# Kernel optimization log

Hardware: AMD Instinct MI355X
Metric: run time of the kernel (lower is better)

Reference implementation:

```python
import jax, jax.numpy as jnp
import numpy as np

N_CHANNELS = 8
SECTION = 32768
F_IN = 64
F_OUT = 64
UNITS = 512


def setup_inputs() -> dict:
    key = jax.random.key(0)
    ks = jax.random.split(key, 10)
    scale = lambda fan_in: 1.0 / np.sqrt(fan_in)
    return {
        "x": jax.random.normal(ks[0], (N_CHANNELS * SECTION, F_IN), jnp.float32),
        "w0": jax.random.normal(ks[1], (N_CHANNELS, UNITS, F_IN), jnp.float32) * scale(F_IN),
        "w1": jax.random.normal(ks[2], (N_CHANNELS, UNITS, UNITS), jnp.float32) * scale(UNITS),
        "w2": jax.random.normal(ks[3], (N_CHANNELS, UNITS, UNITS), jnp.float32) * scale(UNITS),
        "w3": jax.random.normal(ks[4], (N_CHANNELS, F_OUT, UNITS), jnp.float32) * scale(UNITS),
        "b0": jax.random.normal(ks[5], (N_CHANNELS, UNITS), jnp.float32) * 0.01,
        "b1": jax.random.normal(ks[6], (N_CHANNELS, UNITS), jnp.float32) * 0.01,
        "b2": jax.random.normal(ks[7], (N_CHANNELS, UNITS), jnp.float32) * 0.01,
        "b3": jax.random.normal(ks[8], (N_CHANNELS, F_OUT), jnp.float32) * 0.01,
        "section_size": SECTION,
    }


def reference(x, w0, w1, w2, w3, b0, b1, b2, b3, section_size):
    # Equal sections of size `section_size` per channel: reshape to [C, S, F]
    # and run the per-channel MLP as batched (grouped) GEMMs.
    C = w0.shape[0]
    xs = x.reshape(C, section_size, -1)  # [C, S, F_in]
    for w, b in ((w0, b0), (w1, b1), (w2, b2)):
        xs = jax.nn.relu(jnp.einsum('csi,coi->cso', xs, w) + b[:, None, :])
    ys = jnp.einsum('csi,coi->cso', xs, w3) + b3[:, None, :]  # [C, S, F_out]
    return ys.reshape(C * section_size, -1)
```

## Files before the change

### kernel.cpp

```cpp
#include <hip/hip_runtime.h>
#include <hip/hip_bf16.h>

#define CH 8
#define SEC 32768
#define FIN 64
#define FOUT 64
#define UN 512
#define BM 64

typedef __bf16 bf16;
typedef bf16 bf16x8 __attribute__((ext_vector_type(8)));
typedef bf16 bf16x4 __attribute__((ext_vector_type(4)));
typedef float f32x4 __attribute__((ext_vector_type(4)));

__device__ __forceinline__ void gload_lds16(const void* g, void* l) {
  __builtin_amdgcn_global_load_lds(
      (const __attribute__((address_space(1))) void*)g,
      (__attribute__((address_space(3))) void*)l, 16, 0, 0);
}

template<int N>
__device__ __forceinline__ void wait_vmcnt() {
  asm volatile("s_waitcnt vmcnt(%0)" :: "i"(N) : "memory");
  __builtin_amdgcn_sched_barrier(0);
}

__device__ __forceinline__ bf16x8 cvt8(const float* __restrict__ src) {
  f32x4 u0 = *(const f32x4*)src;
  f32x4 u1 = *(const f32x4*)(src + 4);
  bf16x8 v;
  v[0] = (bf16)u0[0]; v[1] = (bf16)u0[1]; v[2] = (bf16)u0[2]; v[3] = (bf16)u0[3];
  v[4] = (bf16)u1[0]; v[5] = (bf16)u1[1]; v[6] = (bf16)u1[2]; v[7] = (bf16)u1[3];
  return v;
}

__device__ __forceinline__ void store_cvt8(void* dst, const float* __restrict__ src) {
  *(bf16x8*)dst = cvt8(src);
}

template<int K, bool WSPATH>
__device__ __forceinline__ void run_main_layer(
    const bf16* __restrict__ wb,
    const float* __restrict__ wf,
    const float* __restrict__ bias, char* __restrict__ act,
    char* __restrict__ wslot,
    int w, int l, int l15, int l4, int rot)
{
  constexpr int NKS = K / 32;
  constexpr int MASK = NKS - 1;
  const int col0 = w * 64;
  const char* abase = act + l * 16;

  f32x4 acc[4][4];
#pragma unroll
  for (int mt = 0; mt < 4; ++mt)
#pragma unroll
    for (int nt = 0; nt < 4; ++nt)
      acc[mt][nt] = f32x4{0.f, 0.f, 0.f, 0.f};

  if constexpr (WSPATH) {
    const bf16* gbase = wb + ((size_t)(w * 4) * NKS * 64 + l) * 8;

    auto stage = [&](int j, int soff) {
      const int ks = (j + rot) & MASK;
#pragma unroll
      for (int i = 0; i < 4; ++i)
        gload_lds16(gbase + (size_t)(i * NKS + ks) * 512, wslot + soff + i * 1024);
    };

    auto compute = [&](int j, int boff) {
      const int ks = (j + rot) & MASK;
      bf16x8 a[4], b[4];
#pragma unroll
      for (int nt = 0; nt < 4; ++nt)
        b[nt] = *(const bf16x8*)(wslot + boff + nt * 1024 + l * 16);
#pragma unroll
      for (int mt = 0; mt < 4; ++mt)
        a[mt] = *(const bf16x8*)(abase + (mt * NKS + ks) * 1024);
      __builtin_amdgcn_s_setprio(1);
#pragma unroll
      for (int mt = 0; mt < 4; ++mt)
#pragma unroll
        for (int nt = 0; nt < 4; ++nt)
          acc[mt][nt] = __builtin_amdgcn_mfma_f32_16x16x32_bf16(a[mt], b[nt], acc[mt][nt], 0, 0, 0);
      __builtin_amdgcn_s_setprio(0);
    };

    stage(0, 0);
    if constexpr (NKS > 1) stage(1, 4096);

    int soff = 8192, boff = 0;
    for (int j = 0; j + 2 < NKS; ++j) {
      stage(j + 2, soff);
      soff += 4096; if (soff == 12288) soff = 0;
      wait_vmcnt<8>();
      compute(j, boff);
      boff += 4096; if (boff == 12288) boff = 0;
    }
    if constexpr (NKS > 1) {
      wait_vmcnt<4>();
      compute(NKS - 2, ((NKS - 2) % 3) * 4096);
    }
    wait_vmcnt<0>();
    compute(NKS - 1, ((NKS - 1) % 3) * 4096);
  } else {
    const float* bpf[4];
#pragma unroll
    for (int nt = 0; nt < 4; ++nt)
      bpf[nt] = wf + (size_t)(col0 + nt * 16 + l15) * K + l4 * 8;
    for (int j = 0; j < NKS; ++j) {
      const int ks = (j + rot) & MASK;
      bf16x8 a[4], b[4];
#pragma unroll
      for (int nt = 0; nt < 4; ++nt) b[nt] = cvt8(bpf[nt] + ks * 32);
#pragma unroll
      for (int mt = 0; mt < 4; ++mt)
        a[mt] = *(const bf16x8*)(abase + (mt * NKS + ks) * 1024);
#pragma unroll
      for (int mt = 0; mt < 4; ++mt)
#pragma unroll
        for (int nt = 0; nt < 4; ++nt)
          acc[mt][nt] = __builtin_amdgcn_mfma_f32_16x16x32_bf16(a[mt], b[nt], acc[mt][nt], 0, 0, 0);
    }
  }

  __syncthreads();

#pragma unroll
  for (int nt = 0; nt < 4; ++nt) {
    const int col = col0 + nt * 16 + l15;
    const float bv = bias[col];
    const int base = (col >> 5) * 1024 + ((col >> 3) & 3) * 256 + (col & 7) * 2 + l4 * 64;
#pragma unroll
    for (int mt = 0; mt < 4; ++mt)
#pragma unroll
      for (int r = 0; r < 4; ++r) {
        float v = acc[mt][nt][r] + bv;
        v = v > 0.f ? v : 0.f;
        *(bf16*)(act + mt * 16384 + base + r * 16) = (bf16)v;
      }
  }
  __syncthreads();
}

template<bool WSPATH>
__device__ __forceinline__ void run_final_layer(
    const bf16* __restrict__ wb, const float* __restrict__ wf,
    const float* __restrict__ bias, const char* __restrict__ act,
    float* __restrict__ gout,
    int w, int l, int l15, int l4, int rot)
{
  constexpr int NKS = 16;
  const int mt = w >> 1;
  const int nb = (w & 1) * 2;
  const char* abase = act + mt * 16384 + l * 16;

  f32x4 acc[2];
  acc[0] = f32x4{0.f, 0.f, 0.f, 0.f};
  acc[1] = f32x4{0.f, 0.f, 0.f, 0.f};

  if constexpr (WSPATH) {
    const bf16* bp0 = wb + ((size_t)(nb + 0) * 16 * 64 + l) * 8;
    const bf16* bp1 = wb + ((size_t)(nb + 1) * 16 * 64 + l) * 8;
    bf16x8 B0[2], B1[2];
    B0[0] = *(const bf16x8*)(bp0 + (size_t)(rot & 15) * 512);
    B0[1] = *(const bf16x8*)(bp1 + (size_t)(rot & 15) * 512);
#pragma unroll
    for (int j = 0; j < NKS; j += 2) {
      {
        const int ksn = (j + 1 + rot) & 15;
        B1[0] = *(const bf16x8*)(bp0 + (size_t)ksn * 512);
        B1[1] = *(const bf16x8*)(bp1 + (size_t)ksn * 512);
        const int ks = (j + rot) & 15;
        const bf16x8 a = *(const bf16x8*)(abase + ks * 1024);
        acc[0] = __builtin_amdgcn_mfma_f32_16x16x32_bf16(a, B0[0], acc[0], 0, 0, 0);
        acc[1] = __builtin_amdgcn_mfma_f32_16x16x32_bf16(a, B0[1], acc[1], 0, 0, 0);
      }
      {
        if (j + 2 < NKS) {
          const int ksn = (j + 2 + rot) & 15;
          B0[0] = *(const bf16x8*)(bp0 + (size_t)ksn * 512);
          B0[1] = *(const bf16x8*)(bp1 + (size_t)ksn * 512);
        }
        const int ks = (j + 1 + rot) & 15;
        const bf16x8 a = *(const bf16x8*)(abase + ks * 1024);
        acc[0] = __builtin_amdgcn_mfma_f32_16x16x32_bf16(a, B1[0], acc[0], 0, 0, 0);
        acc[1] = __builtin_amdgcn_mfma_f32_16x16x32_bf16(a, B1[1], acc[1], 0, 0, 0);
      }
    }
  } else {
    const float* bpf0 = wf + (size_t)((nb + 0) * 16 + l15) * UN + l4 * 8;
    const float* bpf1 = wf + (size_t)((nb + 1) * 16 + l15) * UN + l4 * 8;
    for (int j = 0; j < NKS; ++j) {
      const int ks = (j + rot) & 15;
      const bf16x8 b0 = cvt8(bpf0 + ks * 32);
      const bf16x8 b1 = cvt8(bpf1 + ks * 32);
      const bf16x8 a = *(const bf16x8*)(abase + ks * 1024);
      acc[0] = __builtin_amdgcn_mfma_f32_16x16x32_bf16(a, b0, acc[0], 0, 0, 0);
      acc[1] = __builtin_amdgcn_mfma_f32_16x16x32_bf16(a, b1, acc[1], 0, 0, 0);
    }
  }

#pragma unroll
  for (int i = 0; i < 2; ++i) {
    const int col = (nb + i) * 16 + l15;
    const float bv = bias[col];
#pragma unroll
    for (int r = 0; r < 4; ++r)
      gout[(size_t)(mt * 16 + l4 * 4 + r) * FOUT + col] = acc[i][r] + bv;
  }
}

template<bool WSPATH>
__global__ __launch_bounds__(512, 2) void mlp_fused(
    const float* __restrict__ x,
    const float* __restrict__ w0f, const float* __restrict__ w1f,
    const float* __restrict__ w2f, const float* __restrict__ w3f,
    const float* __restrict__ b0, const float* __restrict__ b1,
    const float* __restrict__ b2, const float* __restrict__ b3,
    const bf16* __restrict__ wbase,
    float* __restrict__ out)
{
  extern __shared__ char smem[];
  char* act = smem;

  const int tid = threadIdx.x;
  const int w = tid >> 6, l = tid & 63;
  const int l15 = l & 15, l4 = l >> 4;
  char* wslot = smem + 65536 + w * 12288;

  const int wg = (blockIdx.x & 7) * 512 + (blockIdx.x >> 3);
  const int ch = wg >> 9;
  const int row0 = (wg & 511) * BM;
  const int rot = wg & 15;

  const bf16* w0b = wbase + (size_t)ch * UN * FIN;
  const bf16* w1b = wbase + CH * UN * FIN + (size_t)ch * UN * UN;
  const bf16* w2b = wbase + CH * UN * FIN + CH * UN * UN + (size_t)ch * UN * UN;
  const bf16* w3b = wbase + CH * UN * FIN + 2 * CH * UN * UN + (size_t)ch * FOUT * UN;
  const float* w0c = w0f + (size_t)ch * UN * FIN;
  const float* w1c = w1f + (size_t)ch * UN * UN;
  const float* w2c = w2f + (size_t)ch * UN * UN;
  const float* w3c = w3f + (size_t)ch * FOUT * UN;
  const float* b0c = b0 + ch * UN;
  const float* b1c = b1 + ch * UN;
  const float* b2c = b2 + ch * UN;
  const float* b3c = b3 + ch * FOUT;

  {
    const float* xs = x + (size_t)(ch * SEC + row0) * FIN;
    store_cvt8(act + w * 1024 + l * 16,
               xs + ((w >> 1) * 16 + l15) * FIN + (w & 1) * 32 + l4 * 8);
  }
  __syncthreads();

  run_main_layer<64,  WSPATH>(w0b, w0c, b0c, act, wslot, w, l, l15, l4, rot);
  run_main_layer<512, WSPATH>(w1b, w1c, b1c, act, wslot, w, l, l15, l4, rot);
  run_main_layer<512, WSPATH>(w2b, w2c, b2c, act, wslot, w, l, l15, l4, rot);
  run_final_layer<WSPATH>(w3b, w3c, b3c, act,
                          out + (size_t)(ch * SEC + row0) * FOUT,
                          w, l, l15, l4, rot);
}

template<int K, int N>
__device__ __forceinline__ void cvt_one(const float* __restrict__ src,
                                        bf16* __restrict__ dst, int t)
{
  constexpr int NKS = K / 32;
  constexpr int perCh = N * K / 8;
  const int ch = t / perCh;
  const int r = t - ch * perCh;
  const int l = r & 63;
  const int p = r >> 6;
  const int ks = p & (NKS - 1);
  const int f = p / NKS;
  const float* s = src + (size_t)ch * N * K + (size_t)(f * 16 + (l & 15)) * K
                 + ks * 32 + (l >> 4) * 8;
  store_cvt8(dst + (size_t)t * 8, s);
}

__global__ void cvt_weights(const float* __restrict__ w0, const float* __restrict__ w1,
                            const float* __restrict__ w2, const float* __restrict__ w3,
                            bf16* __restrict__ o)
{
  constexpr int T0 = CH * UN * FIN / 8;
  constexpr int T1 = CH * UN * UN / 8;
  constexpr int total = 2 * T0 + 2 * T1;
  for (int t = blockIdx.x * blockDim.x + threadIdx.x; t < total;
       t += gridDim.x * blockDim.x) {
    if (t < T0)                cvt_one<FIN, UN>(w0, o, t);
    else if (t < T0 + T1)      cvt_one<UN, UN>(w1, o + CH * UN * FIN, t - T0);
    else if (t < T0 + 2 * T1)  cvt_one<UN, UN>(w2, o + CH * UN * FIN + CH * UN * UN, t - T0 - T1);
    else                       cvt_one<UN, FOUT>(w3, o + CH * UN * FIN + 2 * CH * UN * UN, t - T0 - 2 * T1);
  }
}

extern "C" void kernel_launch(void* const* d_in, const int* in_sizes, int n_in,
                              void* d_out, int out_size, void* d_ws, size_t ws_size,
                              hipStream_t stream)
{
  const float* x  = (const float*)d_in[0];
  const float* w0 = (const float*)d_in[1];
  const float* w1 = (const float*)d_in[2];
  const float* w2 = (const float*)d_in[3];
  const float* w3 = (const float*)d_in[4];
  const float* b0 = (const float*)d_in[5];
  const float* b1 = (const float*)d_in[6];
  const float* b2 = (const float*)d_in[7];
  const float* b3 = (const float*)d_in[8];
  float* out = (float*)d_out;

  const int grid = CH * (SEC / BM);
  const size_t wbytes = (size_t)(2 * CH * UN * FIN + 2 * CH * UN * UN) * 2;

  if (ws_size >= wbytes) {
    bf16* wb = (bf16*)d_ws;
    hipLaunchKernelGGL(cvt_weights, dim3(2304), dim3(256), 0, stream, w0, w1, w2, w3, wb);
    hipFuncSetAttribute(reinterpret_cast<const void*>(mlp_fused<true>),
                        hipFuncAttributeMaxDynamicSharedMemorySize, 163840);
    hipLaunchKernelGGL(mlp_fused<true>, dim3(grid), dim3(512), 163840, stream,
                       x, w0, w1, w2, w3, b0, b1, b2, b3, wb, out);
  } else {
    hipFuncSetAttribute(reinterpret_cast<const void*>(mlp_fused<false>),
                        hipFuncAttributeMaxDynamicSharedMemorySize, 163840);
    hipLaunchKernelGGL(mlp_fused<false>, dim3(grid), dim3(512), 163840, stream,
                       x, w0, w1, w2, w3, b0, b1, b2, b3, (const bf16*)nullptr, out);
  }
}
```

Baseline: 338.1 us.

## Load weights directly to registers with double buffering instead of LDS staging

Replaces the per-wave triple-buffered global-to-LDS weight staging (global_load_lds plus vmcnt waits) with direct global-to-register loads, double-buffered across two register sets and fully unrolled. This removes the 96 KB of per-wave LDS weight slots, cutting dynamic shared memory from 160 KB to 64 KB, which could allow more workgroups per CU. In exchange it raises register pressure and relies on the compiler to schedule the global loads so their latency overlaps with the MFMAs.

```diff
diff --git a/kernel.cpp b/kernel.cpp
--- a/kernel.cpp
+++ b/kernel.cpp
@@ -12,18 +12,6 @@
 typedef bf16 bf16x8 __attribute__((ext_vector_type(8)));
 typedef bf16 bf16x4 __attribute__((ext_vector_type(4)));
 typedef float f32x4 __attribute__((ext_vector_type(4)));
-
-__device__ __forceinline__ void gload_lds16(const void* g, void* l) {
-  __builtin_amdgcn_global_load_lds(
-      (const __attribute__((address_space(1))) void*)g,
-      (__attribute__((address_space(3))) void*)l, 16, 0, 0);
-}
-
-template<int N>
-__device__ __forceinline__ void wait_vmcnt() {
-  asm volatile("s_waitcnt vmcnt(%0)" :: "i"(N) : "memory");
-  __builtin_amdgcn_sched_barrier(0);
-}
 
 __device__ __forceinline__ bf16x8 cvt8(const float* __restrict__ src) {
   f32x4 u0 = *(const f32x4*)src;
@@ -43,7 +31,6 @@
     const bf16* __restrict__ wb,
     const float* __restrict__ wf,
     const float* __restrict__ bias, char* __restrict__ act,
-    char* __restrict__ wslot,
     int w, int l, int l15, int l4, int rot)
 {
   constexpr int NKS = K / 32;
@@ -59,50 +46,57 @@
       acc[mt][nt] = f32x4{0.f, 0.f, 0.f, 0.f};
 
   if constexpr (WSPATH) {
-    const bf16* gbase = wb + ((size_t)(w * 4) * NKS * 64 + l) * 8;
-
-    auto stage = [&](int j, int soff) {
-      const int ks = (j + rot) & MASK;
+    const bf16* bp = wb + ((size_t)(w * 4) * NKS * 64 + l) * 8;
+
+    bf16x8 B0[4], B1[4];
+    {
+      const int ks0 = rot & MASK;
 #pragma unroll
       for (int i = 0; i < 4; ++i)
-        gload_lds16(gbase + (size_t)(i * NKS + ks) * 512, wslot + soff + i * 1024);
-    };
-
-    auto compute = [&](int j, int boff) {
-      const int ks = (j + rot) & MASK;
-      bf16x8 a[4], b[4];
-#pragma unroll
-      for (int nt = 0; nt < 4; ++nt)
-        b[nt] = *(const bf16x8*)(wslot + boff + nt * 1024 + l * 16);
-#pragma unroll
-      for (int mt = 0; mt < 4; ++mt)
-        a[mt] = *(const bf16x8*)(abase + (mt * NKS + ks) * 1024);
-      __builtin_amdgcn_s_setprio(1);
-#pragma unroll
-      for (int mt = 0; mt < 4; ++mt)
-#pragma unroll
-        for (int nt = 0; nt < 4; ++nt)
-          acc[mt][nt] = __builtin_amdgcn_mfma_f32_16x16x32_bf16(a[mt], b[nt], acc[mt][nt], 0, 0, 0);
-      __builtin_amdgcn_s_setprio(0);
-    };
-
-    stage(0, 0);
-    if constexpr (NKS > 1) stage(1, 4096);
-
-    int soff = 8192, boff = 0;
-    for (int j = 0; j + 2 < NKS; ++j) {
-      stage(j + 2, soff);
-      soff += 4096; if (soff == 12288) soff = 0;
-      wait_vmcnt<8>();
-      compute(j, boff);
-      boff += 4096; if (boff == 12288) boff = 0;
-    }
-    if constexpr (NKS > 1) {
-      wait_vmcnt<4>();
-      compute(NKS - 2, ((NKS - 2) % 3) * 4096);
-    }
-    wait_vmcnt<0>();
-    compute(NKS - 1, ((NKS - 1) % 3) * 4096);
+        B0[i] = *(const bf16x8*)(bp + ((size_t)i * NKS + ks0) * 512);
+    }
+
+#pragma unroll
+    for (int j = 0; j < NKS; j += 2) {
+      {
+        const int ksn = (j + 1 + rot) & MASK;
+#pragma unroll
+        for (int i = 0; i < 4; ++i)
+          B1[i] = *(const bf16x8*)(bp + ((size_t)i * NKS + ksn) * 512);
+        const int ks = (j + rot) & MASK;
+        bf16x8 a[4];
+#pragma unroll
+        for (int mt = 0; mt < 4; ++mt)
+          a[mt] = *(const bf16x8*)(abase + (mt * NKS + ks) * 1024);
+        __builtin_amdgcn_s_setprio(1);
+#pragma unroll
+        for (int mt = 0; mt < 4; ++mt)
+#pragma unroll
+          for (int nt = 0; nt < 4; ++nt)
+            acc[mt][nt] = __builtin_amdgcn_mfma_f32_16x16x32_bf16(a[mt], B0[nt], acc[mt][nt], 0, 0, 0);
+        __builtin_amdgcn_s_setprio(0);
+      }
+      {
+        if (j + 2 < NKS) {
+          const int ksn = (j + 2 + rot) & MASK;
+#pragma unroll
+          for (int i = 0; i < 4; ++i)
+            B0[i] = *(const bf16x8*)(bp + ((size_t)i * NKS + ksn) * 512);
+        }
+        const int ks = (j + 1 + rot) & MASK;
+        bf16x8 a[4];
+#pragma unroll
+        for (int mt = 0; mt < 4; ++mt)
+          a[mt] = *(const bf16x8*)(abase + (mt * NKS + ks) * 1024);
+        __builtin_amdgcn_s_setprio(1);
+#pragma unroll
+        for (int mt = 0; mt < 4; ++mt)
+#pragma unroll
+          for (int nt = 0; nt < 4; ++nt)
+            acc[mt][nt] = __builtin_amdgcn_mfma_f32_16x16x32_bf16(a[mt], B1[nt], acc[mt][nt], 0, 0, 0);
+        __builtin_amdgcn_s_setprio(0);
+      }
+    }
   } else {
     const float* bpf[4];
 #pragma unroll
@@ -227,7 +221,6 @@
   const int tid = threadIdx.x;
   const int w = tid >> 6, l = tid & 63;
   const int l15 = l & 15, l4 = l >> 4;
-  char* wslot = smem + 65536 + w * 12288;
 
   const int wg = (blockIdx.x & 7) * 512 + (blockIdx.x >> 3);
   const int ch = wg >> 9;
@@ -254,9 +247,9 @@
   }
   __syncthreads();
 
-  run_main_layer<64,  WSPATH>(w0b, w0c, b0c, act, wslot, w, l, l15, l4, rot);
-  run_main_layer<512, WSPATH>(w1b, w1c, b1c, act, wslot, w, l, l15, l4, rot);
-  run_main_layer<512, WSPATH>(w2b, w2c, b2c, act, wslot, w, l, l15, l4, rot);
+  run_main_layer<64,  WSPATH>(w0b, w0c, b0c, act, w, l, l15, l4, rot);
+  run_main_layer<512, WSPATH>(w1b, w1c, b1c, act, w, l, l15, l4, rot);
+  run_main_layer<512, WSPATH>(w2b, w2c, b2c, act, w, l, l15, l4, rot);
   run_final_layer<WSPATH>(w3b, w3c, b3c, act,
                           out + (size_t)(ch * SEC + row0) * FOUT,
                           w, l, l15, l4, rot);
@@ -317,13 +310,13 @@
     bf16* wb = (bf16*)d_ws;
     hipLaunchKernelGGL(cvt_weights, dim3(2304), dim3(256), 0, stream, w0, w1, w2, w3, wb);
     hipFuncSetAttribute(reinterpret_cast<const void*>(mlp_fused<true>),
-                        hipFuncAttributeMaxDynamicSharedMemorySize, 163840);
-    hipLaunchKernelGGL(mlp_fused<true>, dim3(grid), dim3(512), 163840, stream,
+                        hipFuncAttributeMaxDynamicSharedMemorySize, 65536);
+    hipLaunchKernelGGL(mlp_fused<true>, dim3(grid), dim3(512), 65536, stream,
                        x, w0, w1, w2, w3, b0, b1, b2, b3, wb, out);
   } else {
     hipFuncSetAttribute(reinterpret_cast<const void*>(mlp_fused<false>),
-                        hipFuncAttributeMaxDynamicSharedMemorySize, 163840);
-    hipLaunchKernelGGL(mlp_fused<false>, dim3(grid), dim3(512), 163840, stream,
+                        hipFuncAttributeMaxDynamicSharedMemorySize, 65536);
+    hipLaunchKernelGGL(mlp_fused<false>, dim3(grid), dim3(512), 65536, stream,
                        x, w0, w1, w2, w3, b0, b1, b2, b3, (const bf16*)nullptr, out);
   }
 }
```

Result: faster. 309.5 us (-8.5%).
